# Optimization experiments

Measured on AMD Instinct MI355X. Metric: run time of the kernel, lower is better.

## Reference

```python
import jax, jax.numpy as jnp
import numpy as np

N_ORDERS = 4  # edge groups processed sequentially by EmulsionConv


def setup_inputs() -> dict:
    key = jax.random.key(0)
    ks = jax.random.split(key, 12)
    N, E, D_IN, H, D_OUT, ED = 50000, 800000, 10, 64, 10, 1
    s = 0.1
    return {
        "x": jax.random.normal(ks[0], (N, D_IN), jnp.float32),
        "edge_index": jax.random.randint(ks[1], (2, E), 0, N, jnp.int32),
        "edge_features": jax.random.normal(ks[2], (E, ED), jnp.float32),
        "lin0_w": jax.random.normal(ks[3], (D_IN, H), jnp.float32) * s,
        "lin0_b": jnp.zeros((H,), jnp.float32),
        "lin1_w": jax.random.normal(ks[4], (H, H), jnp.float32) * s,
        "lin1_b": jnp.zeros((H,), jnp.float32),
        "lin2_w": jax.random.normal(ks[5], (H, H), jnp.float32) * s,
        "lin2_b": jnp.zeros((H,), jnp.float32),
        "em_w": jax.random.normal(ks[6], (3, 2 * H + ED, H), jnp.float32) * s,
        "em_b": jnp.zeros((3, H), jnp.float32),
        "ec_w": jax.random.normal(ks[7], (3, 2 * H, H), jnp.float32) * s,
        "ec_b": jnp.zeros((3, H), jnp.float32),
        "out_w": jax.random.normal(ks[8], (H, D_OUT), jnp.float32) * s,
        "out_b": jnp.zeros((D_OUT,), jnp.float32),
    }


def _emulsion_conv(x, edge_index, edge_features, w, b):
    # Sequential per-order gather -> MLP message -> scatter-add; direction=0 (aggregate at source).
    N = x.shape[0]
    E = edge_index.shape[1]
    per = E // N_ORDERS
    for i in range(N_ORDERS):
        sl = slice(i * per, (i + 1) * per)
        src = edge_index[0, sl]
        dst = edge_index[1, sl]
        x_j = x[src]  # [per, H]
        x_i = x[dst]  # [per, H]
        msg = jnp.concatenate([x_i, x_j - x_i, edge_features[sl]], axis=1)
        msg = jax.nn.relu(msg @ w + b)
        agg = jax.ops.segment_sum(msg, src, num_segments=N)
        x = (x + agg) / 2.0
    return x


def _edge_conv(x, edge_index, w, b):
    # EdgeConv: nn([x_i, x_j - x_i]) with max aggregation at target nodes.
    N = x.shape[0]
    src, dst = edge_index[0], edge_index[1]
    x_i = x[dst]
    x_j = x[src]
    msg = jax.nn.relu(jnp.concatenate([x_i, x_j - x_i], axis=1) @ w + b)
    agg = jax.ops.segment_max(msg, dst, num_segments=N)
    return jnp.where(jnp.isfinite(agg), agg, 0.0)  # empty segments -> 0


def reference(x, edge_index, edge_features,
              lin0_w, lin0_b, lin1_w, lin1_b, lin2_w, lin2_b,
              em_w, em_b, ec_w, ec_b, out_w, out_b):
    lin_ws = [lin0_w, lin1_w, lin2_w]
    lin_bs = [lin0_b, lin1_b, lin2_b]
    for i in range(3):
        x = jax.nn.relu(x @ lin_ws[i] + lin_bs[i])
        x = _emulsion_conv(x, edge_index, edge_features, em_w[i], em_b[i])
    for i in range(3):
        x = _edge_conv(x, edge_index, ec_w[i], ec_b[i])
    return x @ out_w + out_b
```

## Files before the change

kernel.cpp:

```cpp
#include <hip/hip_runtime.h>
#include <hip/hip_fp16.h>


#define NN 50000
#define NE 800000
#define PER 200000
#define HD 64
#define NKEY 250112

typedef _Float16 half8 __attribute__((ext_vector_type(8)));
typedef float float4v __attribute__((ext_vector_type(4)));

__global__ __launch_bounds__(256) void count_kernel(
        const int* __restrict__ ei, int* __restrict__ cnt,
        uchar2* __restrict__ rank) {
    int e = blockIdx.x * 256 + threadIdx.x;
    if (e >= NE) return;
    int src = ei[e];
    int dst = ei[NE + e];
    int o = e / PER;
    int r1 = atomicAdd(&cnt[o * NN + src], 1);
    int r2 = atomicAdd(&cnt[4 * NN + dst], 1);
    rank[e] = make_uchar2((unsigned char)r1, (unsigned char)r2);
}

__global__ __launch_bounds__(256) void scan_blk(
        const int* __restrict__ cnt, int* __restrict__ bsum) {
    __shared__ int s[256];
    int t = threadIdx.x;
    int i = blockIdx.x * 256 + t;
    int c = (i < NKEY) ? cnt[i] : 0;
    s[t] = c; __syncthreads();
    for (int d = 1; d < 256; d <<= 1) {
        int v = (t >= d) ? s[t - d] : 0;
        __syncthreads(); s[t] += v; __syncthreads();
    }
    if (t == 255) bsum[blockIdx.x] = s[255];
}

__global__ __launch_bounds__(1024) void scan_top(
        const int* __restrict__ bsum, int* __restrict__ bofs, int nb) {
    __shared__ int s[1024];
    int t = threadIdx.x;
    int c = (t < nb) ? bsum[t] : 0;
    s[t] = c; __syncthreads();
    for (int d = 1; d < 1024; d <<= 1) {
        int v = (t >= d) ? s[t - d] : 0;
        __syncthreads(); s[t] += v; __syncthreads();
    }
    if (t < nb) bofs[t] = s[t] - c;
}

__global__ __launch_bounds__(256) void scan_fin(
        const int* __restrict__ cnt, const int* __restrict__ bofs,
        int* __restrict__ ofs) {
    __shared__ int s[256];
    int t = threadIdx.x;
    int i = blockIdx.x * 256 + t;
    int c = (i < NKEY) ? cnt[i] : 0;
    s[t] = c; __syncthreads();
    for (int d = 1; d < 256; d <<= 1) {
        int v = (t >= d) ? s[t - d] : 0;
        __syncthreads(); s[t] += v; __syncthreads();
    }
    if (i < NKEY) ofs[i] = bofs[blockIdx.x] + s[t] - c;
}

__global__ __launch_bounds__(256) void fill_kernel(
        const int* __restrict__ ei, const float* __restrict__ ef,
        const int* __restrict__ ofs, const uchar2* __restrict__ rank,
        unsigned* __restrict__ em_val, int* __restrict__ ec_val) {
    int e = blockIdx.x * 256 + threadIdx.x;
    if (e >= NE) return;
    int src = ei[e];
    int dst = ei[NE + e];
    int o = e / PER;
    uchar2 r = rank[e];
    int p1 = ofs[o * NN + src] + r.x;
    unsigned short eb = __half_as_ushort(__float2half_rn(ef[e]));
    em_val[p1] = ((unsigned)dst << 16) | (unsigned)eb;
    int p2 = ofs[4 * NN + dst] + r.y - NE;
    ec_val[p2] = src;
}

__global__ __launch_bounds__(256) void prep_w(
        const float* __restrict__ em_w, const float* __restrict__ ec_w,
        _Float16* __restrict__ wh) {
    int idx = blockIdx.x * 256 + threadIdx.x;
    int mat = idx >> 12, pos = idx & 4095;
    int n = pos >> 6, k = pos & 63;
    float val;
    if (mat < 3)      { const float* B = em_w + mat * 129 * 64;     val = B[k*64+n] - B[(64+k)*64+n]; }
    else if (mat < 6) { const float* B = em_w + (mat-3) * 129 * 64; val = B[(64+k)*64+n]; }
    else if (mat < 9) { const float* B = ec_w + (mat-6) * 128 * 64; val = B[k*64+n] - B[(64+k)*64+n]; }
    else              { const float* B = ec_w + (mat-9) * 128 * 64; val = B[(64+k)*64+n]; }
    _Float16 h = (_Float16)val;
    _Float16 l = (_Float16)(val - (float)h);
    wh[(size_t)mat * 4096 + n * 64 + k] = h;
    wh[(size_t)(12 + mat) * 4096 + n * 64 + k] = l;
}

template<int K>
__global__ __launch_bounds__(256) void lin_kernel(
        const float* __restrict__ xin,
        const float* __restrict__ W, const float* __restrict__ bias,
        float* __restrict__ xout) {
    __shared__ float xs[64][K + 1];
    int t = threadIdx.x;
    int n0 = blockIdx.x * 64;
    for (int idx = t; idx < 64 * K; idx += 256) {
        int n = idx / K, k = idx - n * K;
        int g = n0 + n;
        xs[n][k] = (g < NN) ? xin[(size_t)g * K + k] : 0.f;
    }
    __syncthreads();
    int ng = t >> 4;
    int f0 = (t & 15) * 4;
    float acc[4][4] = {};
    for (int k = 0; k < K; ++k) {
        float4 w4 = *(const float4*)&W[k * HD + f0];
        #pragma unroll
        for (int j = 0; j < 4; ++j) {
            float xv = xs[ng * 4 + j][k];
            acc[j][0] += xv * w4.x; acc[j][1] += xv * w4.y;
            acc[j][2] += xv * w4.z; acc[j][3] += xv * w4.w;
        }
    }
    float4 b4 = *(const float4*)&bias[f0];
    #pragma unroll
    for (int j = 0; j < 4; ++j) {
        int g = n0 + ng * 4 + j;
        if (g < NN) {
            float4 o;
            o.x = fmaxf(acc[j][0] + b4.x, 0.f);
            o.y = fmaxf(acc[j][1] + b4.y, 0.f);
            o.z = fmaxf(acc[j][2] + b4.z, 0.f);
            o.w = fmaxf(acc[j][3] + b4.w, 0.f);
            *(float4*)&xout[(size_t)g * HD + f0] = o;
        }
    }
}

__global__ __launch_bounds__(256) void uv_mfma(
        const float* __restrict__ x,
        const _Float16* __restrict__ Wuh, const _Float16* __restrict__ Wul,
        const _Float16* __restrict__ Wvh, const _Float16* __restrict__ Wvl,
        const float* __restrict__ bias,
        _Float16* __restrict__ u, _Float16* __restrict__ v) {
    __shared__ _Float16 xh[64 * 72], xl[64 * 72];
    __shared__ _Float16 wuh[64 * 72], wul[64 * 72];
    __shared__ _Float16 wvh[64 * 72], wvl[64 * 72];
    __shared__ _Float16 rp[4 * 16 * 72];
    int t = threadIdx.x;
    int n0 = blockIdx.x * 64;

    {
        int node = t >> 2, k0 = (t & 3) * 16;
        int g = n0 + node;
        float f[16];
        if (g < NN) {
            const float4* xr = (const float4*)&x[(size_t)g * HD + k0];
            *(float4*)&f[0] = xr[0]; *(float4*)&f[4] = xr[1];
            *(float4*)&f[8] = xr[2]; *(float4*)&f[12] = xr[3];
        } else {
            #pragma unroll
            for (int j = 0; j < 16; ++j) f[j] = 0.f;
        }
        half8 h0, h1, l0, l1;
        #pragma unroll
        for (int j = 0; j < 8; ++j) {
            _Float16 h = (_Float16)f[j];
            h0[j] = h; l0[j] = (_Float16)(f[j] - (float)h);
            _Float16 g2 = (_Float16)f[j + 8];
            h1[j] = g2; l1[j] = (_Float16)(f[j + 8] - (float)g2);
        }
        *(half8*)&xh[node * 72 + k0] = h0; *(half8*)&xh[node * 72 + k0 + 8] = h1;
        *(half8*)&xl[node * 72 + k0] = l0; *(half8*)&xl[node * 72 + k0 + 8] = l1;
    }
    {
        int n = t >> 2, c = (t & 3) * 16;
        *(half8*)&wuh[n * 72 + c]     = *(const half8*)&Wuh[n * 64 + c];
        *(half8*)&wuh[n * 72 + c + 8] = *(const half8*)&Wuh[n * 64 + c + 8];
        *(half8*)&wul[n * 72 + c]     = *(const half8*)&Wul[n * 64 + c];
        *(half8*)&wul[n * 72 + c + 8] = *(const half8*)&Wul[n * 64 + c + 8];
        *(half8*)&wvh[n * 72 + c]     = *(const half8*)&Wvh[n * 64 + c];
        *(half8*)&wvh[n * 72 + c + 8] = *(const half8*)&Wvh[n * 64 + c + 8];
        *(half8*)&wvl[n * 72 + c]     = *(const half8*)&Wvl[n * 64 + c];
        *(half8*)&wvl[n * 72 + c + 8] = *(const half8*)&Wvl[n * 64 + c + 8];
    }
    __syncthreads();

    int w = t >> 6, lane = t & 63;
    int quad = lane >> 4, l16 = lane & 15;
    int m0 = w * 16;
    half8 ah0 = *(half8*)&xh[(m0 + l16) * 72 + quad * 8];
    half8 ah1 = *(half8*)&xh[(m0 + l16) * 72 + 32 + quad * 8];
    half8 al0 = *(half8*)&xl[(m0 + l16) * 72 + quad * 8];
    half8 al1 = *(half8*)&xl[(m0 + l16) * 72 + 32 + quad * 8];

    float4v au[4], av[4];
    #pragma unroll
    for (int nt = 0; nt < 4; ++nt) {
        int n = nt * 16 + l16;
        half8 bh0 = *(half8*)&wuh[n * 72 + quad * 8];
        half8 bh1 = *(half8*)&wuh[n * 72 + 32 + quad * 8];
        half8 bl0 = *(half8*)&wul[n * 72 + quad * 8];
        half8 bl1 = *(half8*)&wul[n * 72 + 32 + quad * 8];
        float4v acc = {0.f, 0.f, 0.f, 0.f};
        acc = __builtin_amdgcn_mfma_f32_16x16x32_f16(ah0, bh0, acc, 0, 0, 0);
        acc = __builtin_amdgcn_mfma_f32_16x16x32_f16(ah1, bh1, acc, 0, 0, 0);
        acc = __builtin_amdgcn_mfma_f32_16x16x32_f16(al0, bh0, acc, 0, 0, 0);
        acc = __builtin_amdgcn_mfma_f32_16x16x32_f16(al1, bh1, acc, 0, 0, 0);
        acc = __builtin_amdgcn_mfma_f32_16x16x32_f16(ah0, bl0, acc, 0, 0, 0);
        acc = __builtin_amdgcn_mfma_f32_16x16x32_f16(ah1, bl1, acc, 0, 0, 0);
        au[nt] = acc;
        half8 ch0 = *(half8*)&wvh[n * 72 + quad * 8];
        half8 ch1 = *(half8*)&wvh[n * 72 + 32 + quad * 8];
        half8 cl0 = *(half8*)&wvl[n * 72 + quad * 8];
        half8 cl1 = *(half8*)&wvl[n * 72 + 32 + quad * 8];
        float4v accv = {0.f, 0.f, 0.f, 0.f};
        accv = __builtin_amdgcn_mfma_f32_16x16x32_f16(ah0, ch0, accv, 0, 0, 0);
        accv = __builtin_amdgcn_mfma_f32_16x16x32_f16(ah1, ch1, accv, 0, 0, 0);
        accv = __builtin_amdgcn_mfma_f32_16x16x32_f16(al0, ch0, accv, 0, 0, 0);
        accv = __builtin_amdgcn_mfma_f32_16x16x32_f16(al1, ch1, accv, 0, 0, 0);
        accv = __builtin_amdgcn_mfma_f32_16x16x32_f16(ah0, cl0, accv, 0, 0, 0);
        accv = __builtin_amdgcn_mfma_f32_16x16x32_f16(ah1, cl1, accv, 0, 0, 0);
        av[nt] = accv;
    }

    _Float16* rpw = &rp[w * 16 * 72];
    #pragma unroll
    for (int nt = 0; nt < 4; ++nt) {
        float bn = bias[nt * 16 + l16];
        #pragma unroll
        for (int r = 0; r < 4; ++r)
            rpw[(quad * 4 + r) * 72 + nt * 16 + l16] = (_Float16)(au[nt][r] + bn);
    }
    int mr = lane >> 2, cr = (lane & 3) * 16;
    int gr = n0 + m0 + mr;
    if (gr < NN) {
        *(half8*)&u[(size_t)gr * HD + cr]     = *(half8*)&rpw[mr * 72 + cr];
        *(half8*)&u[(size_t)gr * HD + cr + 8] = *(half8*)&rpw[mr * 72 + cr + 8];
    }
    #pragma unroll
    for (int nt = 0; nt < 4; ++nt) {
        #pragma unroll
        for (int r = 0; r < 4; ++r)
            rpw[(quad * 4 + r) * 72 + nt * 16 + l16] = (_Float16)(av[nt][r]);
    }
    if (gr < NN) {
        *(half8*)&v[(size_t)gr * HD + cr]     = *(half8*)&rpw[mr * 72 + cr];
        *(half8*)&v[(size_t)gr * HD + cr + 8] = *(half8*)&rpw[mr * 72 + cr + 8];
    }
}

__device__ __forceinline__ void load_h8(const __half* p, float* o) {
    float4 r = *(const float4*)p;
    __half2 h0 = *reinterpret_cast<__half2*>(&r.x);
    __half2 h1 = *reinterpret_cast<__half2*>(&r.y);
    __half2 h2 = *reinterpret_cast<__half2*>(&r.z);
    __half2 h3 = *reinterpret_cast<__half2*>(&r.w);
    float2 f0 = __half22float2(h0), f1 = __half22float2(h1);
    float2 f2 = __half22float2(h2), f3 = __half22float2(h3);
    o[0] = f0.x; o[1] = f0.y; o[2] = f1.x; o[3] = f1.y;
    o[4] = f2.x; o[5] = f2.y; o[6] = f3.x; o[7] = f3.y;
}

__global__ __launch_bounds__(256) void em_edge(
        const unsigned* __restrict__ em_val, const int* __restrict__ ofs,
        const __half* __restrict__ u, const __half* __restrict__ v,
        const float* __restrict__ we, float* __restrict__ x, int order) {
    int t = threadIdx.x;
    int node = blockIdx.x * 32 + (t >> 3);
    if (node >= NN) return;
    int f0 = (t & 7) * 8;
    int key = order * NN + node;
    int s0 = ofs[key], s1 = ofs[key + 1];
    float vn[8], wef[8], acc[8] = {};
    load_h8(&v[(size_t)node * HD + f0], vn);
    *(float4*)&wef[0] = *(const float4*)&we[f0];
    *(float4*)&wef[4] = *(const float4*)&we[f0 + 4];
    int p = s0;
    for (; p + 2 <= s1; p += 2) {
        unsigned e0 = em_val[p], e1 = em_val[p + 1];
        float u0[8], u1[8];
        load_h8(&u[(size_t)(e0 >> 16) * HD + f0], u0);
        load_h8(&u[(size_t)(e1 >> 16) * HD + f0], u1);
        float ef0 = __half2float(__ushort_as_half((unsigned short)(e0 & 0xffff)));
        float ef1 = __half2float(__ushort_as_half((unsigned short)(e1 & 0xffff)));
        #pragma unroll
        for (int j = 0; j < 8; ++j) {
            acc[j] += fmaxf(u0[j] + vn[j] + ef0 * wef[j], 0.f)
                    + fmaxf(u1[j] + vn[j] + ef1 * wef[j], 0.f);
        }
    }
    if (p < s1) {
        unsigned e0 = em_val[p];
        float u0[8];
        load_h8(&u[(size_t)(e0 >> 16) * HD + f0], u0);
        float ef0 = __half2float(__ushort_as_half((unsigned short)(e0 & 0xffff)));
        #pragma unroll
        for (int j = 0; j < 8; ++j)
            acc[j] += fmaxf(u0[j] + vn[j] + ef0 * wef[j], 0.f);
    }
    float xr[8];
    *(float4*)&xr[0] = *(const float4*)&x[(size_t)node * HD + f0];
    *(float4*)&xr[4] = *(const float4*)&x[(size_t)node * HD + f0 + 4];
    #pragma unroll
    for (int j = 0; j < 8; ++j) xr[j] = (xr[j] + acc[j]) * 0.5f;
    *(float4*)&x[(size_t)node * HD + f0] = *(float4*)&xr[0];
    *(float4*)&x[(size_t)node * HD + f0 + 4] = *(float4*)&xr[4];
}

__global__ __launch_bounds__(256) void ec_edge(
        const int* __restrict__ ec_val, const int* __restrict__ ofs,
        const __half* __restrict__ u, const __half* __restrict__ v,
        float* __restrict__ x) {
    int t = threadIdx.x;
    int node = blockIdx.x * 32 + (t >> 3);
    if (node >= NN) return;
    int f0 = (t & 7) * 8;
    int s0 = ofs[4 * NN + node] - NE, s1 = ofs[4 * NN + node + 1] - NE;
    float un[8], m[8] = {};
    load_h8(&u[(size_t)node * HD + f0], un);
    int p = s0;
    for (; p + 2 <= s1; p += 2) {
        int i0 = ec_val[p], i1 = ec_val[p + 1];
        float v0[8], v1[8];
        load_h8(&v[(size_t)i0 * HD + f0], v0);
        load_h8(&v[(size_t)i1 * HD + f0], v1);
        #pragma unroll
        for (int j = 0; j < 8; ++j)
            m[j] = fmaxf(m[j], fmaxf(un[j] + v0[j], un[j] + v1[j]));
    }
    if (p < s1) {
        int i0 = ec_val[p];
        float v0[8];
        load_h8(&v[(size_t)i0 * HD + f0], v0);
        #pragma unroll
        for (int j = 0; j < 8; ++j) m[j] = fmaxf(m[j], un[j] + v0[j]);
    }
    *(float4*)&x[(size_t)node * HD + f0] = *(float4*)&m[0];
    *(float4*)&x[(size_t)node * HD + f0 + 4] = *(float4*)&m[4];
}

__global__ __launch_bounds__(256) void out_kernel(
        const float* __restrict__ x, const float* __restrict__ W,
        const float* __restrict__ bias, float* __restrict__ out) {
    int n = blockIdx.x * 256 + threadIdx.x;
    if (n >= NN) return;
    float xr[HD];
    #pragma unroll
    for (int k = 0; k < HD; k += 4) {
        float4 t4 = *(const float4*)&x[(size_t)n * HD + k];
        xr[k] = t4.x; xr[k + 1] = t4.y; xr[k + 2] = t4.z; xr[k + 3] = t4.w;
    }
    #pragma unroll
    for (int f = 0; f < 10; ++f) {
        float acc = bias[f];
        #pragma unroll
        for (int k = 0; k < HD; ++k) acc += xr[k] * W[k * 10 + f];
        out[(size_t)n * 10 + f] = acc;
    }
}

extern "C" void kernel_launch(void* const* d_in, const int* in_sizes, int n_in,
                              void* d_out, int out_size, void* d_ws, size_t ws_size,
                              hipStream_t stream) {
    const float* x_in  = (const float*)d_in[0];
    const int*   ei    = (const int*)d_in[1];
    const float* ef    = (const float*)d_in[2];
    const float* lw[3] = {(const float*)d_in[3], (const float*)d_in[5], (const float*)d_in[7]};
    const float* lb[3] = {(const float*)d_in[4], (const float*)d_in[6], (const float*)d_in[8]};
    const float* em_w  = (const float*)d_in[9];
    const float* em_b  = (const float*)d_in[10];
    const float* ec_w  = (const float*)d_in[11];
    const float* ec_b  = (const float*)d_in[12];
    const float* ow    = (const float*)d_in[13];
    const float* ob    = (const float*)d_in[14];
    float* out = (float*)d_out;

    char* wsb = (char*)d_ws;
    size_t off = 0;
    auto alloc = [&](size_t bytes) {
        void* p = wsb + off;
        off = (off + bytes + 255) & ~(size_t)255;
        return p;
    };
    float*     x      = (float*)alloc((size_t)NN * HD * 4);
    _Float16*  u      = (_Float16*)alloc((size_t)NN * HD * 2);
    _Float16*  v      = (_Float16*)alloc((size_t)NN * HD * 2);
    int*       cnt    = (int*)alloc((size_t)NKEY * 4);
    int*       ofs    = (int*)alloc((size_t)NKEY * 4);
    int*       bsum   = (int*)alloc((size_t)1024 * 4);
    int*       bofs   = (int*)alloc((size_t)1024 * 4);
    uchar2*    rank   = (uchar2*)alloc((size_t)NE * 2);
    unsigned*  em_val = (unsigned*)alloc((size_t)NE * 4);
    int*       ec_val = (int*)alloc((size_t)NE * 4);
    _Float16*  wh     = (_Float16*)alloc((size_t)24 * 4096 * 2);
    (void)ws_size; (void)in_sizes; (void)n_in; (void)out_size;

    const int gb_nodes = (NN + 63) / 64;
    const int gb_edges = (NE + 255) / 256;
    const int gb_n8    = (NN + 31) / 32;
    const int gb_keys  = NKEY / 256;

    hipMemsetAsync(cnt, 0, (size_t)NKEY * 4, stream);
    count_kernel<<<gb_edges, 256, 0, stream>>>(ei, cnt, rank);
    prep_w<<<192, 256, 0, stream>>>(em_w, ec_w, wh);
    scan_blk<<<gb_keys, 256, 0, stream>>>(cnt, bsum);
    scan_top<<<1, 1024, 0, stream>>>(bsum, bofs, gb_keys);
    scan_fin<<<gb_keys, 256, 0, stream>>>(cnt, bofs, ofs);
    fill_kernel<<<gb_edges, 256, 0, stream>>>(ei, ef, ofs, rank, em_val, ec_val);

    lin_kernel<10><<<gb_nodes, 256, 0, stream>>>(x_in, lw[0], lb[0], x);

    for (int i = 0; i < 3; ++i) {
        const _Float16* Wuh = wh + (size_t)i * 4096;
        const _Float16* Wvh = wh + (size_t)(3 + i) * 4096;
        const _Float16* Wul = wh + (size_t)(12 + i) * 4096;
        const _Float16* Wvl = wh + (size_t)(15 + i) * 4096;
        const float* bi = em_b + (size_t)i * HD;
        const float* we = em_w + (size_t)i * 129 * HD + 128 * HD;
        for (int o = 0; o < 4; ++o) {
            uv_mfma<<<gb_nodes, 256, 0, stream>>>(x, Wuh, Wul, Wvh, Wvl, bi, u, v);
            em_edge<<<gb_n8, 256, 0, stream>>>(em_val, ofs, (const __half*)u,
                                               (const __half*)v, we, x, o);
        }
        if (i < 2)
            lin_kernel<64><<<gb_nodes, 256, 0, stream>>>(x, lw[i + 1], lb[i + 1], x);
    }

    for (int j = 0; j < 3; ++j) {
        const _Float16* Wuh = wh + (size_t)(6 + j) * 4096;
        const _Float16* Wvh = wh + (size_t)(9 + j) * 4096;
        const _Float16* Wul = wh + (size_t)(18 + j) * 4096;
        const _Float16* Wvl = wh + (size_t)(21 + j) * 4096;
        const float* bj = ec_b + (size_t)j * HD;
        uv_mfma<<<gb_nodes, 256, 0, stream>>>(x, Wuh, Wul, Wvh, Wvl, bj, u, v);
        ec_edge<<<gb_n8, 256, 0, stream>>>(ec_val, ofs, (const __half*)u,
                                           (const __half*)v, x);
    }

    out_kernel<<<(NN + 255) / 256, 256, 0, stream>>>(x, ow, ob, out);
}
```

Measured before the change: 579.2 us.

## Pad atomic counters, partition CSR fill by XCD, shrink uv_mfma LDS

```diff
diff --git a/kernel.cpp b/kernel.cpp
--- a/kernel.cpp
+++ b/kernel.cpp
@@ -7,6 +7,7 @@
 #define PER 200000
 #define HD 64
 #define NKEY 250112
+#define CSTR 8
 
 typedef _Float16 half8 __attribute__((ext_vector_type(8)));
 typedef float float4v __attribute__((ext_vector_type(4)));
@@ -19,8 +20,8 @@
     int src = ei[e];
     int dst = ei[NE + e];
     int o = e / PER;
-    int r1 = atomicAdd(&cnt[o * NN + src], 1);
-    int r2 = atomicAdd(&cnt[4 * NN + dst], 1);
+    int r1 = atomicAdd(&cnt[(o * NN + src) * CSTR], 1);
+    int r2 = atomicAdd(&cnt[(4 * NN + dst) * CSTR], 1);
     rank[e] = make_uchar2((unsigned char)r1, (unsigned char)r2);
 }
 
@@ -29,7 +30,7 @@
     __shared__ int s[256];
     int t = threadIdx.x;
     int i = blockIdx.x * 256 + t;
-    int c = (i < NKEY) ? cnt[i] : 0;
+    int c = (i < NKEY) ? cnt[(size_t)i * CSTR] : 0;
     s[t] = c; __syncthreads();
     for (int d = 1; d < 256; d <<= 1) {
         int v = (t >= d) ? s[t - d] : 0;
@@ -57,7 +58,7 @@
     __shared__ int s[256];
     int t = threadIdx.x;
     int i = blockIdx.x * 256 + t;
-    int c = (i < NKEY) ? cnt[i] : 0;
+    int c = (i < NKEY) ? cnt[(size_t)i * CSTR] : 0;
     s[t] = c; __syncthreads();
     for (int d = 1; d < 256; d <<= 1) {
         int v = (t >= d) ? s[t - d] : 0;
@@ -66,21 +67,28 @@
     if (i < NKEY) ofs[i] = bofs[blockIdx.x] + s[t] - c;
 }
 
-__global__ __launch_bounds__(256) void fill_kernel(
+__global__ __launch_bounds__(256) void fill_xcd(
         const int* __restrict__ ei, const float* __restrict__ ef,
         const int* __restrict__ ofs, const uchar2* __restrict__ rank,
         unsigned* __restrict__ em_val, int* __restrict__ ec_val) {
-    int e = blockIdx.x * 256 + threadIdx.x;
-    if (e >= NE) return;
-    int src = ei[e];
-    int dst = ei[NE + e];
-    int o = e / PER;
-    uchar2 r = rank[e];
-    int p1 = ofs[o * NN + src] + r.x;
-    unsigned short eb = __half_as_ushort(__float2half_rn(ef[e]));
-    em_val[p1] = ((unsigned)dst << 16) | (unsigned)eb;
-    int p2 = ofs[4 * NN + dst] + r.y - NE;
-    ec_val[p2] = src;
+    int cls = blockIdx.x & 7;
+    int base = (blockIdx.x >> 3) * (NE / 128);
+    for (int i = threadIdx.x; i < NE / 128; i += 256) {
+        int e = base + i;
+        int src = ei[e];
+        int dst = ei[NE + e];
+        uchar2 r = rank[e];
+        if (((src >> 3) & 7) == cls) {
+            int o = e / PER;
+            int p1 = ofs[o * NN + src] + r.x;
+            unsigned short eb = __half_as_ushort(__float2half_rn(ef[e]));
+            em_val[p1] = ((unsigned)dst << 16) | (unsigned)eb;
+        }
+        if (((dst >> 3) & 7) == cls) {
+            int p2 = ofs[4 * NN + dst] + r.y - NE;
+            ec_val[p2] = src;
+        }
+    }
 }
 
 __global__ __launch_bounds__(256) void prep_w(
@@ -147,65 +155,70 @@
         const _Float16* __restrict__ Wvh, const _Float16* __restrict__ Wvl,
         const float* __restrict__ bias,
         _Float16* __restrict__ u, _Float16* __restrict__ v) {
-    __shared__ _Float16 xh[64 * 72], xl[64 * 72];
-    __shared__ _Float16 wuh[64 * 72], wul[64 * 72];
-    __shared__ _Float16 wvh[64 * 72], wvl[64 * 72];
-    __shared__ _Float16 rp[4 * 16 * 72];
+    __shared__ __align__(16) char smem[64 * 66 * 4 + 4 * 64 * 68 * 2];
+    float* xs = (float*)smem;
+    _Float16* wlds = (_Float16*)(smem + 64 * 66 * 4);
+    _Float16* rp = (_Float16*)smem;
     int t = threadIdx.x;
     int n0 = blockIdx.x * 64;
 
     {
         int node = t >> 2, k0 = (t & 3) * 16;
         int g = n0 + node;
-        float f[16];
+        float4 f0v, f1v, f2v, f3v;
         if (g < NN) {
             const float4* xr = (const float4*)&x[(size_t)g * HD + k0];
-            *(float4*)&f[0] = xr[0]; *(float4*)&f[4] = xr[1];
-            *(float4*)&f[8] = xr[2]; *(float4*)&f[12] = xr[3];
+            f0v = xr[0]; f1v = xr[1]; f2v = xr[2]; f3v = xr[3];
         } else {
-            #pragma unroll
-            for (int j = 0; j < 16; ++j) f[j] = 0.f;
-        }
-        half8 h0, h1, l0, l1;
-        #pragma unroll
-        for (int j = 0; j < 8; ++j) {
-            _Float16 h = (_Float16)f[j];
-            h0[j] = h; l0[j] = (_Float16)(f[j] - (float)h);
-            _Float16 g2 = (_Float16)f[j + 8];
-            h1[j] = g2; l1[j] = (_Float16)(f[j + 8] - (float)g2);
-        }
-        *(half8*)&xh[node * 72 + k0] = h0; *(half8*)&xh[node * 72 + k0 + 8] = h1;
-        *(half8*)&xl[node * 72 + k0] = l0; *(half8*)&xl[node * 72 + k0 + 8] = l1;
+            f0v = f1v = f2v = f3v = make_float4(0.f, 0.f, 0.f, 0.f);
+        }
+        float* d = &xs[node * 66 + k0];
+        *(float4*)&d[0] = f0v; *(float4*)&d[4] = f1v;
+        *(float4*)&d[8] = f2v; *(float4*)&d[12] = f3v;
     }
     {
-        int n = t >> 2, c = (t & 3) * 16;
-        *(half8*)&wuh[n * 72 + c]     = *(const half8*)&Wuh[n * 64 + c];
-        *(half8*)&wuh[n * 72 + c + 8] = *(const half8*)&Wuh[n * 64 + c + 8];
-        *(half8*)&wul[n * 72 + c]     = *(const half8*)&Wul[n * 64 + c];
-        *(half8*)&wul[n * 72 + c + 8] = *(const half8*)&Wul[n * 64 + c + 8];
-        *(half8*)&wvh[n * 72 + c]     = *(const half8*)&Wvh[n * 64 + c];
-        *(half8*)&wvh[n * 72 + c + 8] = *(const half8*)&Wvh[n * 64 + c + 8];
-        *(half8*)&wvl[n * 72 + c]     = *(const half8*)&Wvl[n * 64 + c];
-        *(half8*)&wvl[n * 72 + c + 8] = *(const half8*)&Wvl[n * 64 + c + 8];
+        int row = t >> 2, c = (t & 3) * 16;
+        const _Float16* srcs[4] = {Wuh, Wul, Wvh, Wvl};
+        #pragma unroll
+        for (int m = 0; m < 4; ++m) {
+            _Float16* d = &wlds[m * 64 * 68 + row * 68 + c];
+            *(half8*)&d[0] = *(const half8*)&srcs[m][row * 64 + c];
+            *(half8*)&d[8] = *(const half8*)&srcs[m][row * 64 + c + 8];
+        }
     }
     __syncthreads();
 
     int w = t >> 6, lane = t & 63;
     int quad = lane >> 4, l16 = lane & 15;
     int m0 = w * 16;
-    half8 ah0 = *(half8*)&xh[(m0 + l16) * 72 + quad * 8];
-    half8 ah1 = *(half8*)&xh[(m0 + l16) * 72 + 32 + quad * 8];
-    half8 al0 = *(half8*)&xl[(m0 + l16) * 72 + quad * 8];
-    half8 al1 = *(half8*)&xl[(m0 + l16) * 72 + 32 + quad * 8];
+    half8 ah0, ah1, al0, al1;
+    {
+        const float* r0 = &xs[(m0 + l16) * 66 + quad * 8];
+        const float* r1 = &xs[(m0 + l16) * 66 + 32 + quad * 8];
+        #pragma unroll
+        for (int j = 0; j < 8; ++j) {
+            float f = r0[j];
+            _Float16 h = (_Float16)f;
+            ah0[j] = h; al0[j] = (_Float16)(f - (float)h);
+            float g2 = r1[j];
+            _Float16 h2 = (_Float16)g2;
+            ah1[j] = h2; al1[j] = (_Float16)(g2 - (float)h2);
+        }
+    }
+    __syncthreads();
 
     float4v au[4], av[4];
     #pragma unroll
     for (int nt = 0; nt < 4; ++nt) {
         int n = nt * 16 + l16;
-        half8 bh0 = *(half8*)&wuh[n * 72 + quad * 8];
-        half8 bh1 = *(half8*)&wuh[n * 72 + 32 + quad * 8];
-        half8 bl0 = *(half8*)&wul[n * 72 + quad * 8];
-        half8 bl1 = *(half8*)&wul[n * 72 + 32 + quad * 8];
+        const _Float16* bu_h = &wlds[0 * 64 * 68 + n * 68];
+        const _Float16* bu_l = &wlds[1 * 64 * 68 + n * 68];
+        const _Float16* bv_h = &wlds[2 * 64 * 68 + n * 68];
+        const _Float16* bv_l = &wlds[3 * 64 * 68 + n * 68];
+        half8 bh0 = *(const half8*)&bu_h[quad * 8];
+        half8 bh1 = *(const half8*)&bu_h[32 + quad * 8];
+        half8 bl0 = *(const half8*)&bu_l[quad * 8];
+        half8 bl1 = *(const half8*)&bu_l[32 + quad * 8];
         float4v acc = {0.f, 0.f, 0.f, 0.f};
         acc = __builtin_amdgcn_mfma_f32_16x16x32_f16(ah0, bh0, acc, 0, 0, 0);
         acc = __builtin_amdgcn_mfma_f32_16x16x32_f16(ah1, bh1, acc, 0, 0, 0);
@@ -214,10 +227,10 @@
         acc = __builtin_amdgcn_mfma_f32_16x16x32_f16(ah0, bl0, acc, 0, 0, 0);
         acc = __builtin_amdgcn_mfma_f32_16x16x32_f16(ah1, bl1, acc, 0, 0, 0);
         au[nt] = acc;
-        half8 ch0 = *(half8*)&wvh[n * 72 + quad * 8];
-        half8 ch1 = *(half8*)&wvh[n * 72 + 32 + quad * 8];
-        half8 cl0 = *(half8*)&wvl[n * 72 + quad * 8];
-        half8 cl1 = *(half8*)&wvl[n * 72 + 32 + quad * 8];
+        half8 ch0 = *(const half8*)&bv_h[quad * 8];
+        half8 ch1 = *(const half8*)&bv_h[32 + quad * 8];
+        half8 cl0 = *(const half8*)&bv_l[quad * 8];
+        half8 cl1 = *(const half8*)&bv_l[32 + quad * 8];
         float4v accv = {0.f, 0.f, 0.f, 0.f};
         accv = __builtin_amdgcn_mfma_f32_16x16x32_f16(ah0, ch0, accv, 0, 0, 0);
         accv = __builtin_amdgcn_mfma_f32_16x16x32_f16(ah1, ch1, accv, 0, 0, 0);
@@ -390,7 +403,7 @@
     float*     x      = (float*)alloc((size_t)NN * HD * 4);
     _Float16*  u      = (_Float16*)alloc((size_t)NN * HD * 2);
     _Float16*  v      = (_Float16*)alloc((size_t)NN * HD * 2);
-    int*       cnt    = (int*)alloc((size_t)NKEY * 4);
+    int*       cnt    = (int*)alloc((size_t)NKEY * CSTR * 4);
     int*       ofs    = (int*)alloc((size_t)NKEY * 4);
     int*       bsum   = (int*)alloc((size_t)1024 * 4);
     int*       bofs   = (int*)alloc((size_t)1024 * 4);
@@ -405,13 +418,13 @@
     const int gb_n8    = (NN + 31) / 32;
     const int gb_keys  = NKEY / 256;
 
-    hipMemsetAsync(cnt, 0, (size_t)NKEY * 4, stream);
+    hipMemsetAsync(cnt, 0, (size_t)NKEY * CSTR * 4, stream);
     count_kernel<<<gb_edges, 256, 0, stream>>>(ei, cnt, rank);
     prep_w<<<192, 256, 0, stream>>>(em_w, ec_w, wh);
     scan_blk<<<gb_keys, 256, 0, stream>>>(cnt, bsum);
     scan_top<<<1, 1024, 0, stream>>>(bsum, bofs, gb_keys);
     scan_fin<<<gb_keys, 256, 0, stream>>>(cnt, bofs, ofs);
-    fill_kernel<<<gb_edges, 256, 0, stream>>>(ei, ef, ofs, rank, em_val, ec_val);
+    fill_xcd<<<1024, 256, 0, stream>>>(ei, ef, ofs, rank, em_val, ec_val);
 
     lin_kernel<10><<<gb_nodes, 256, 0, stream>>>(x_in, lw[0], lb[0], x);
 
```

Measured after the change: 816.6 us. +41.0%, slower.
